# Kernel optimization log

Measured on AMD Instinct MI355X. Metric: run time of the kernel, lower is better.

Reference implementation:

```python
import jax, jax.numpy as jnp
import numpy as np

NEG = -1e30  # finite stand-in for -inf; exp underflows to exactly 0 in fp32


def setup_inputs() -> dict:
    key = jax.random.key(0)
    ks = jax.random.split(key, 8)
    B, L1, L2, D = 32, 2048, 512, 256
    x = jax.random.normal(ks[0], (B, L1, D), dtype=jnp.float32)
    y = jax.random.normal(ks[1], (B, L2, D), dtype=jnp.float32)
    x_mask = jax.random.randint(ks[2], (B, L1), 0, 2) > 0  # True = padding
    y_mask = jax.random.randint(ks[3], (B, L2), 0, 2) > 0
    w_x = jax.random.normal(ks[4], (D, 1), dtype=jnp.float32) * (1.0 / np.sqrt(D))
    w_y = jax.random.normal(ks[5], (D, 1), dtype=jnp.float32) * (1.0 / np.sqrt(D))
    w_dot = jax.random.normal(ks[6], (D, 1), dtype=jnp.float32) * (1.0 / np.sqrt(D))
    bias = jnp.zeros((1,), dtype=jnp.float32)
    return {"x": x, "y": y, "x_mask": x_mask, "y_mask": y_mask,
            "w_x": w_x, "w_y": w_y, "w_dot": w_dot, "bias": bias}


def reference(x, y, x_mask, y_mask, w_x, w_y, w_dot, bias):
    # trilinear BiDAF score: bias + x@w_x + y@w_y + sum_d x_d * y_d * w_dot_d
    # factorized -> no (B,L1,L2,D) intermediate, same math as xy.mm(w_dot)
    sx = x @ w_x                                    # (B, L1, 1)
    sy = jnp.swapaxes(y @ w_y, 1, 2)                # (B, 1, L2)
    sdot = jnp.einsum('bid,bjd->bij', x * w_dot[:, 0], y)  # (B, L1, L2)
    scores = bias[0] + sx + sy + sdot               # (B, L1, L2)
    scores = jnp.where(x_mask[:, :, None], NEG, scores)
    scores = jnp.where(y_mask[:, None, :], NEG, scores)

    alpha = jax.nn.softmax(scores, axis=2)          # (B, L1, L2)
    # torch code sets NaN rows (fully masked x positions) to 0
    valid_x = (~x_mask)[:, :, None].astype(x.dtype)
    alpha = alpha * valid_x
    c2q_attn = jnp.einsum('bij,bjd->bid', alpha, y)  # (B, L1, D)
    c2q_attn = c2q_attn * valid_x                    # maskzero on x padding

    beta = jax.nn.softmax(jnp.max(scores, axis=2), axis=1)  # (B, L1)
    q2c_attn = jnp.einsum('bi,bid->bd', beta, x)[:, None, :]  # (B, 1, D)

    return (c2q_attn, q2c_attn, x * c2q_attn)
```

## Files before the change

### kernel.cpp

```cpp
#include <hip/hip_runtime.h>
#include <stdint.h>

#define BB 32
#define L1 2048
#define L2 512
#define DD 256
#define NEGV -1e30f

typedef __attribute__((ext_vector_type(4))) float f32x4;
typedef __attribute__((ext_vector_type(8))) short bf16x8;
typedef __attribute__((ext_vector_type(4))) unsigned short u16x4;
typedef __attribute__((ext_vector_type(8))) unsigned short u16x8;

__device__ __forceinline__ unsigned short f2bf(float f) {
    unsigned int u = __float_as_uint(f);
    u += 0x7FFFu + ((u >> 16) & 1u);
    return (unsigned short)(u >> 16);
}

__global__ void prep(const float* __restrict__ y, const float* __restrict__ w_y,
                     unsigned short* __restrict__ ybf, unsigned short* __restrict__ yt,
                     float* __restrict__ sy) {
    __shared__ float tile[64][264];
    const int tid = threadIdx.x;
    const int lane = tid & 63;
    const int sub = tid >> 6;
    const int b = blockIdx.y;
    const int j0 = blockIdx.x * 64;
    const float* yb = y + ((size_t)b * L2 + j0) * DD;
    f32x4 wv = *(const f32x4*)(w_y + lane * 4);
    #pragma unroll
    for (int p = 0; p < 16; ++p) {
        int row = p * 4 + sub;
        f32x4 v = *(const f32x4*)(yb + (size_t)row * DD + lane * 4);
        *(f32x4*)&tile[row][lane * 4] = v;
        u16x4 o;
        o[0] = f2bf(v[0]); o[1] = f2bf(v[1]); o[2] = f2bf(v[2]); o[3] = f2bf(v[3]);
        *(u16x4*)(ybf + ((size_t)b * L2 + j0 + row) * DD + lane * 4) = o;
        float s = v[0]*wv[0] + v[1]*wv[1] + v[2]*wv[2] + v[3]*wv[3];
        #pragma unroll
        for (int off = 32; off; off >>= 1) s += __shfl_xor(s, off, 64);
        if (lane == 0) sy[b * L2 + j0 + row] = s;
    }
    __syncthreads();
    #pragma unroll
    for (int p = 0; p < 8; ++p) {
        int d = p * 32 + (tid >> 3);
        int jo = (tid & 7) * 8;
        u16x8 pk;
        #pragma unroll
        for (int jj = 0; jj < 8; ++jj) pk[jj] = f2bf(tile[jo + jj][d]);
        *(u16x8*)(yt + ((size_t)b * DD + d) * L2 + j0 + jo) = pk;
    }
}

__launch_bounds__(256, 2)
__global__ void attn_main(const float* __restrict__ x,
                          const unsigned short* __restrict__ ybf,
                          const unsigned short* __restrict__ yt,
                          const float* __restrict__ sy,
                          const float* __restrict__ w_x,
                          const float* __restrict__ w_dot,
                          const float* __restrict__ bias,
                          const int* __restrict__ x_mask,
                          const int* __restrict__ y_mask,
                          float* __restrict__ out0,
                          float* __restrict__ out2,
                          float* __restrict__ part,
                          float* __restrict__ MbA,
                          float* __restrict__ SeA) {
    __shared__ __align__(16) unsigned short big[32768];
    __shared__ float sxs[64];
    __shared__ int   xms[64];
    __shared__ float pmax[4][64];
    __shared__ float pz[4][64];

    const int tid = threadIdx.x;
    const int w = tid >> 6;
    const int lane = tid & 63;
    const int g = lane >> 4, c = lane & 15;

    const int wg = blockIdx.x;
    const int slot = wg >> 3;
    const int b = (wg & 7) * 4 + (slot >> 5);
    const int rowblk = slot & 31;
    const int i0 = rowblk * 64;

    const int arow = w * 16 + c;
    const float* xrow = x + ((size_t)(b * L1 + i0 + arow)) * DD;
    float sxpart = 0.f;
    #pragma unroll
    for (int kb = 0; kb < 8; ++kb) {
        int koff = kb * 32 + g * 8;
        f32x4 lo = *(const f32x4*)(xrow + koff);
        f32x4 hi = *(const f32x4*)(xrow + koff + 4);
        f32x4 wdlo = *(const f32x4*)(w_dot + koff);
        f32x4 wdhi = *(const f32x4*)(w_dot + koff + 4);
        f32x4 wxlo = *(const f32x4*)(w_x + koff);
        f32x4 wxhi = *(const f32x4*)(w_x + koff + 4);
        u16x8 a;
        #pragma unroll
        for (int e = 0; e < 4; ++e) {
            a[e]     = f2bf(lo[e] * wdlo[e]);
            a[e + 4] = f2bf(hi[e] * wdhi[e]);
            sxpart += lo[e] * wxlo[e] + hi[e] * wxhi[e];
        }
        int u = (kb * 4 + g) ^ (c & 7);
        *(u16x8*)((char*)big + arow * 512 + u * 16) = a;
    }
    sxpart += __shfl_xor(sxpart, 16, 64);
    sxpart += __shfl_xor(sxpart, 32, 64);
    if (g == 0) {
        sxs[arow] = sxpart + bias[0];
        xms[arow] = x_mask[b * L1 + i0 + arow];
    }
    __syncthreads();

    f32x4 S[4][8];
    #pragma unroll
    for (int mt = 0; mt < 4; ++mt)
        #pragma unroll
        for (int nt = 0; nt < 8; ++nt) S[mt][nt] = (f32x4){0.f, 0.f, 0.f, 0.f};

    const unsigned short* ybase = ybf + (size_t)b * L2 * DD;
    const int col0 = w * 128;
    #pragma unroll 2
    for (int ck = 0; ck < 8; ++ck) {
        bf16x8 bfr[8];
        #pragma unroll
        for (int nt = 0; nt < 8; ++nt)
            bfr[nt] = *(const bf16x8*)(ybase + (size_t)(col0 + nt * 16 + c) * DD + ck * 32 + g * 8);
        bf16x8 afr[4];
        #pragma unroll
        for (int mt = 0; mt < 4; ++mt) {
            int u = (ck * 4 + g) ^ (c & 7);
            afr[mt] = *(const bf16x8*)((char*)big + (mt * 16 + c) * 512 + u * 16);
        }
        #pragma unroll
        for (int mt = 0; mt < 4; ++mt)
            #pragma unroll
            for (int nt = 0; nt < 8; ++nt)
                S[mt][nt] = __builtin_amdgcn_mfma_f32_16x16x32_bf16(afr[mt], bfr[nt], S[mt][nt], 0, 0, 0);
    }

    float syv[8]; int ymv[8];
    #pragma unroll
    for (int nt = 0; nt < 8; ++nt) {
        syv[nt] = sy[b * L2 + col0 + nt * 16 + c];
        ymv[nt] = y_mask[b * L2 + col0 + nt * 16 + c];
    }
    float sxr[4][4]; int xmr[4][4];
    #pragma unroll
    for (int mt = 0; mt < 4; ++mt)
        #pragma unroll
        for (int r = 0; r < 4; ++r) {
            sxr[mt][r] = sxs[mt * 16 + 4 * g + r];
            xmr[mt][r] = xms[mt * 16 + 4 * g + r];
        }
    #pragma unroll
    for (int mt = 0; mt < 4; ++mt)
        #pragma unroll
        for (int nt = 0; nt < 8; ++nt)
            #pragma unroll
            for (int r = 0; r < 4; ++r) {
                float v = S[mt][nt][r] + sxr[mt][r] + syv[nt];
                if (ymv[nt]) v = NEGV;
                if (xmr[mt][r]) v = NEGV;
                S[mt][nt][r] = v;
            }

    float mrow[4][4];
    #pragma unroll
    for (int mt = 0; mt < 4; ++mt)
        #pragma unroll
        for (int r = 0; r < 4; ++r) {
            float pm = S[mt][0][r];
            #pragma unroll
            for (int nt = 1; nt < 8; ++nt) pm = fmaxf(pm, S[mt][nt][r]);
            pm = fmaxf(pm, __shfl_xor(pm, 1, 64));
            pm = fmaxf(pm, __shfl_xor(pm, 2, 64));
            pm = fmaxf(pm, __shfl_xor(pm, 4, 64));
            pm = fmaxf(pm, __shfl_xor(pm, 8, 64));
            if (c == 0) pmax[w][mt * 16 + 4 * g + r] = pm;
        }
    __syncthreads();
    #pragma unroll
    for (int mt = 0; mt < 4; ++mt)
        #pragma unroll
        for (int r = 0; r < 4; ++r) {
            int row = mt * 16 + 4 * g + r;
            mrow[mt][r] = fmaxf(fmaxf(pmax[0][row], pmax[1][row]),
                                fmaxf(pmax[2][row], pmax[3][row]));
        }
    #pragma unroll
    for (int mt = 0; mt < 4; ++mt)
        #pragma unroll
        for (int r = 0; r < 4; ++r) {
            float zp = 0.f;
            #pragma unroll
            for (int nt = 0; nt < 8; ++nt) {
                float e = __expf(S[mt][nt][r] - mrow[mt][r]);
                S[mt][nt][r] = e;
                zp += e;
            }
            zp += __shfl_xor(zp, 1, 64);
            zp += __shfl_xor(zp, 2, 64);
            zp += __shfl_xor(zp, 4, 64);
            zp += __shfl_xor(zp, 8, 64);
            if (c == 0) pz[w][mt * 16 + 4 * g + r] = zp;
        }
    __syncthreads();
    float zinv[4][4];
    #pragma unroll
    for (int mt = 0; mt < 4; ++mt)
        #pragma unroll
        for (int r = 0; r < 4; ++r) {
            int row = mt * 16 + 4 * g + r;
            zinv[mt][r] = 1.f / (pz[0][row] + pz[1][row] + pz[2][row] + pz[3][row]);
        }

    float Mb;
    {
        float t = mrow[0][0];
        #pragma unroll
        for (int mt = 0; mt < 4; ++mt)
            #pragma unroll
            for (int r = 0; r < 4; ++r) t = fmaxf(t, mrow[mt][r]);
        t = fmaxf(t, __shfl_xor(t, 16, 64));
        t = fmaxf(t, __shfl_xor(t, 32, 64));
        Mb = t;
    }
    float ev[4][4];
    float Se = 0.f;
    #pragma unroll
    for (int mt = 0; mt < 4; ++mt)
        #pragma unroll
        for (int r = 0; r < 4; ++r) {
            ev[mt][r] = __expf(mrow[mt][r] - Mb);
            Se += ev[mt][r];
        }
    Se += __shfl_xor(Se, 16, 64);
    Se += __shfl_xor(Se, 32, 64);
    if (tid == 0) {
        MbA[b * 32 + rowblk] = Mb;
        SeA[b * 32 + rowblk] = Se;
    }

    #pragma unroll
    for (int mt = 0; mt < 4; ++mt)
        #pragma unroll
        for (int nt = 0; nt < 8; ++nt)
            #pragma unroll
            for (int r = 0; r < 4; ++r) {
                int row = mt * 16 + 4 * g + r;
                int col = col0 + nt * 16 + c;
                *(unsigned short*)((char*)big + row * 1024 +
                                   (((col >> 3) ^ (row & 7)) * 16) + (col & 7) * 2)
                    = f2bf(S[mt][nt][r]);
            }
    __syncthreads();

    f32x4 o[4][4];
    #pragma unroll
    for (int mt = 0; mt < 4; ++mt)
        #pragma unroll
        for (int nt = 0; nt < 4; ++nt) o[mt][nt] = (f32x4){0.f, 0.f, 0.f, 0.f};
    const unsigned short* ytb = yt + (size_t)b * DD * L2;
    const int d0 = w * 64;
    #pragma unroll 4
    for (int kf = 0; kf < 16; ++kf) {
        bf16x8 bv[4];
        #pragma unroll
        for (int nt = 0; nt < 4; ++nt)
            bv[nt] = *(const bf16x8*)(ytb + (size_t)(d0 + nt * 16 + c) * L2 + kf * 32 + g * 8);
        bf16x8 av[4];
        #pragma unroll
        for (int mt = 0; mt < 4; ++mt) {
            int u = (kf * 4 + g) ^ (c & 7);
            av[mt] = *(const bf16x8*)((char*)big + (mt * 16 + c) * 1024 + u * 16);
        }
        #pragma unroll
        for (int mt = 0; mt < 4; ++mt)
            #pragma unroll
            for (int nt = 0; nt < 4; ++nt)
                o[mt][nt] = __builtin_amdgcn_mfma_f32_16x16x32_bf16(av[mt], bv[nt], o[mt][nt], 0, 0, 0);
    }

    const float* xb2 = x + ((size_t)b * L1 + i0) * DD;
    const size_t outb = ((size_t)b * L1 + i0) * DD;
    float eq[4] = {0.f, 0.f, 0.f, 0.f};
    #pragma unroll
    for (int mt = 0; mt < 4; ++mt)
        #pragma unroll
        for (int r = 0; r < 4; ++r) {
            int row = mt * 16 + 4 * g + r;
            float zi = zinv[mt][r];
            float ee = ev[mt][r];
            int xmv = xmr[mt][r];
            #pragma unroll
            for (int nt = 0; nt < 4; ++nt) {
                int d = d0 + nt * 16 + c;
                float xv = xb2[(size_t)row * DD + d];
                float cv = xmv ? 0.f : o[mt][nt][r] * zi;
                out0[outb + (size_t)row * DD + d] = cv;
                out2[outb + (size_t)row * DD + d] = xv * cv;
                eq[nt] += ee * xv;
            }
        }
    #pragma unroll
    for (int nt = 0; nt < 4; ++nt) {
        float v = eq[nt];
        v += __shfl_xor(v, 16, 64);
        v += __shfl_xor(v, 32, 64);
        if (g == 0) part[((size_t)(b * 32 + rowblk)) * DD + d0 + nt * 16 + c] = v;
    }
}

__global__ void q2c_combine(const float* __restrict__ part, const float* __restrict__ MbA,
                            const float* __restrict__ SeA, float* __restrict__ out1) {
    int b = blockIdx.x, d = threadIdx.x;
    float M = -3.0e38f;
    #pragma unroll
    for (int k = 0; k < 32; ++k) M = fmaxf(M, MbA[b * 32 + k]);
    float Z = 0.f, s = 0.f;
    #pragma unroll
    for (int k = 0; k < 32; ++k) {
        float wk = __expf(MbA[b * 32 + k] - M);
        Z += SeA[b * 32 + k] * wk;
        s += part[((size_t)(b * 32 + k)) * DD + d] * wk;
    }
    out1[b * DD + d] = s / Z;
}

extern "C" void kernel_launch(void* const* d_in, const int* in_sizes, int n_in,
                              void* d_out, int out_size, void* d_ws, size_t ws_size,
                              hipStream_t stream) {
    const float* x = (const float*)d_in[0];
    const float* y = (const float*)d_in[1];
    const int* x_mask = (const int*)d_in[2];
    const int* y_mask = (const int*)d_in[3];
    const float* w_x = (const float*)d_in[4];
    const float* w_y = (const float*)d_in[5];
    const float* w_dot = (const float*)d_in[6];
    const float* bias = (const float*)d_in[7];

    char* ws = (char*)d_ws;
    unsigned short* ybf = (unsigned short*)ws;
    unsigned short* yt  = (unsigned short*)(ws + 8388608);
    float* sy   = (float*)(ws + 16777216);
    float* part = (float*)(ws + 16842752);
    float* MbA  = (float*)(ws + 17891328);
    float* SeA  = (float*)(ws + 17895424);

    float* out0 = (float*)d_out;
    float* out1 = out0 + (size_t)BB * L1 * DD;
    float* out2 = out1 + (size_t)BB * DD;

    prep<<<dim3(L2 / 64, BB), 256, 0, stream>>>(y, w_y, ybf, yt, sy);
    attn_main<<<dim3(BB * L1 / 64), 256, 0, stream>>>(x, ybf, yt, sy, w_x, w_dot, bias,
                                                      x_mask, y_mask, out0, out2,
                                                      part, MbA, SeA);
    q2c_combine<<<dim3(BB), 256, 0, stream>>>(part, MbA, SeA, out1);
}
```

Before: 124.3 us.

## Halve attention row tile to 32 rows, use exp2 with pre-scaled scores

Shrinks each workgroup's row tile from 64 to 32, which halves the LDS footprint and the register accumulators. The launch-bounds occupancy hint goes from 2 to 3, the grid doubles, and q2c_combine now reduces over 64 partials. Scores are pre-scaled by log2(e) so the softmax can use the hardware exp2, and the masks are folded into the sx/sy bias terms as large negatives, replacing the per-element selects. The cost is that each workgroup reloads the full bf16 y tiles, so global/L2 traffic for y doubles, and the bf16 conversion now uses the library intrinsic.

```diff
diff --git a/kernel.cpp b/kernel.cpp
--- a/kernel.cpp
+++ b/kernel.cpp
@@ -1,21 +1,29 @@
 #include <hip/hip_runtime.h>
+#include <hip/hip_bf16.h>
 #include <stdint.h>
 
 #define BB 32
 #define L1 2048
 #define L2 512
 #define DD 256
-#define NEGV -1e30f
+#define L2E 1.4426950408889634f
+#define NEGS (-1.0e30f * 1.4426950408889634f)
+
+#if __has_builtin(__builtin_amdgcn_exp2f)
+#define EXP2(x) __builtin_amdgcn_exp2f(x)
+#else
+#define EXP2(x) exp2f(x)
+#endif
 
 typedef __attribute__((ext_vector_type(4))) float f32x4;
 typedef __attribute__((ext_vector_type(8))) short bf16x8;
 typedef __attribute__((ext_vector_type(4))) unsigned short u16x4;
 typedef __attribute__((ext_vector_type(8))) unsigned short u16x8;
 
-__device__ __forceinline__ unsigned short f2bf(float f) {
-    unsigned int u = __float_as_uint(f);
-    u += 0x7FFFu + ((u >> 16) & 1u);
-    return (unsigned short)(u >> 16);
+__device__ __forceinline__ unsigned short f2b(float f) {
+    union { __hip_bfloat16 h; unsigned short u; } cv;
+    cv.h = __float2bfloat16(f);
+    return cv.u;
 }
 
 __global__ void prep(const float* __restrict__ y, const float* __restrict__ w_y,
@@ -35,7 +43,7 @@
         f32x4 v = *(const f32x4*)(yb + (size_t)row * DD + lane * 4);
         *(f32x4*)&tile[row][lane * 4] = v;
         u16x4 o;
-        o[0] = f2bf(v[0]); o[1] = f2bf(v[1]); o[2] = f2bf(v[2]); o[3] = f2bf(v[3]);
+        o[0] = f2b(v[0]); o[1] = f2b(v[1]); o[2] = f2b(v[2]); o[3] = f2b(v[3]);
         *(u16x4*)(ybf + ((size_t)b * L2 + j0 + row) * DD + lane * 4) = o;
         float s = v[0]*wv[0] + v[1]*wv[1] + v[2]*wv[2] + v[3]*wv[3];
         #pragma unroll
@@ -49,12 +57,12 @@
         int jo = (tid & 7) * 8;
         u16x8 pk;
         #pragma unroll
-        for (int jj = 0; jj < 8; ++jj) pk[jj] = f2bf(tile[jo + jj][d]);
+        for (int jj = 0; jj < 8; ++jj) pk[jj] = f2b(tile[jo + jj][d]);
         *(u16x8*)(yt + ((size_t)b * DD + d) * L2 + j0 + jo) = pk;
     }
 }
 
-__launch_bounds__(256, 2)
+__launch_bounds__(256, 3)
 __global__ void attn_main(const float* __restrict__ x,
                           const unsigned short* __restrict__ ybf,
                           const unsigned short* __restrict__ yt,
@@ -69,11 +77,11 @@
                           float* __restrict__ part,
                           float* __restrict__ MbA,
                           float* __restrict__ SeA) {
-    __shared__ __align__(16) unsigned short big[32768];
-    __shared__ float sxs[64];
-    __shared__ int   xms[64];
-    __shared__ float pmax[4][64];
-    __shared__ float pz[4][64];
+    __shared__ __align__(16) unsigned short big[16384];
+    __shared__ float sxs[32];
+    __shared__ int   xms[32];
+    __shared__ float pmax[4][32];
+    __shared__ float pz[4][32];
 
     const int tid = threadIdx.x;
     const int w = tid >> 6;
@@ -82,96 +90,90 @@
 
     const int wg = blockIdx.x;
     const int slot = wg >> 3;
-    const int b = (wg & 7) * 4 + (slot >> 5);
-    const int rowblk = slot & 31;
-    const int i0 = rowblk * 64;
-
-    const int arow = w * 16 + c;
-    const float* xrow = x + ((size_t)(b * L1 + i0 + arow)) * DD;
-    float sxpart = 0.f;
-    #pragma unroll
-    for (int kb = 0; kb < 8; ++kb) {
-        int koff = kb * 32 + g * 8;
-        f32x4 lo = *(const f32x4*)(xrow + koff);
-        f32x4 hi = *(const f32x4*)(xrow + koff + 4);
-        f32x4 wdlo = *(const f32x4*)(w_dot + koff);
-        f32x4 wdhi = *(const f32x4*)(w_dot + koff + 4);
-        f32x4 wxlo = *(const f32x4*)(w_x + koff);
-        f32x4 wxhi = *(const f32x4*)(w_x + koff + 4);
-        u16x8 a;
-        #pragma unroll
-        for (int e = 0; e < 4; ++e) {
-            a[e]     = f2bf(lo[e] * wdlo[e]);
-            a[e + 4] = f2bf(hi[e] * wdhi[e]);
-            sxpart += lo[e] * wxlo[e] + hi[e] * wxhi[e];
-        }
-        int u = (kb * 4 + g) ^ (c & 7);
-        *(u16x8*)((char*)big + arow * 512 + u * 16) = a;
-    }
-    sxpart += __shfl_xor(sxpart, 16, 64);
-    sxpart += __shfl_xor(sxpart, 32, 64);
-    if (g == 0) {
-        sxs[arow] = sxpart + bias[0];
-        xms[arow] = x_mask[b * L1 + i0 + arow];
-    }
-    __syncthreads();
-
-    f32x4 S[4][8];
-    #pragma unroll
-    for (int mt = 0; mt < 4; ++mt)
+    const int b = (wg & 7) * 4 + (slot >> 6);
+    const int rowblk = slot & 63;
+    const int i0 = rowblk * 32;
+
+    {
+        const int arow = w * 8 + (lane >> 3);
+        const int chunk = lane & 7;
+        const float* xr = x + ((size_t)(b * L1 + i0 + arow)) * DD + chunk * 32;
+        const float* wdp = w_dot + chunk * 32;
+        const float* wxp = w_x + chunk * 32;
+        float sxp = 0.f;
+        #pragma unroll
+        for (int it = 0; it < 8; ++it) {
+            f32x4 xv = *(const f32x4*)(xr + it * 4);
+            f32x4 wdv = *(const f32x4*)(wdp + it * 4);
+            f32x4 wxv = *(const f32x4*)(wxp + it * 4);
+            u16x4 a;
+            #pragma unroll
+            for (int e = 0; e < 4; ++e) a[e] = f2b(xv[e] * wdv[e]);
+            sxp += xv[0]*wxv[0] + xv[1]*wxv[1] + xv[2]*wxv[2] + xv[3]*wxv[3];
+            int gr = chunk * 4 + (it >> 1);
+            *(u16x4*)((char*)big + arow * 512 + ((gr ^ (arow & 7)) << 4) + (it & 1) * 8) = a;
+        }
+        sxp += __shfl_xor(sxp, 1, 64);
+        sxp += __shfl_xor(sxp, 2, 64);
+        sxp += __shfl_xor(sxp, 4, 64);
+        if (chunk == 0) {
+            int xmv = x_mask[b * L1 + i0 + arow];
+            xms[arow] = xmv;
+            sxs[arow] = xmv ? NEGS : (sxp + bias[0]) * L2E;
+        }
+    }
+    __syncthreads();
+
+    f32x4 S[2][8];
+    #pragma unroll
+    for (int mt = 0; mt < 2; ++mt)
         #pragma unroll
         for (int nt = 0; nt < 8; ++nt) S[mt][nt] = (f32x4){0.f, 0.f, 0.f, 0.f};
 
     const unsigned short* ybase = ybf + (size_t)b * L2 * DD;
     const int col0 = w * 128;
-    #pragma unroll 2
+    #pragma unroll
     for (int ck = 0; ck < 8; ++ck) {
         bf16x8 bfr[8];
         #pragma unroll
         for (int nt = 0; nt < 8; ++nt)
             bfr[nt] = *(const bf16x8*)(ybase + (size_t)(col0 + nt * 16 + c) * DD + ck * 32 + g * 8);
-        bf16x8 afr[4];
-        #pragma unroll
-        for (int mt = 0; mt < 4; ++mt) {
-            int u = (ck * 4 + g) ^ (c & 7);
-            afr[mt] = *(const bf16x8*)((char*)big + (mt * 16 + c) * 512 + u * 16);
-        }
-        #pragma unroll
-        for (int mt = 0; mt < 4; ++mt)
+        bf16x8 afr[2];
+        #pragma unroll
+        for (int mt = 0; mt < 2; ++mt)
+            afr[mt] = *(const bf16x8*)((char*)big + (mt * 16 + c) * 512 + ((((ck * 4 + g)) ^ (c & 7)) << 4));
+        #pragma unroll
+        for (int mt = 0; mt < 2; ++mt)
             #pragma unroll
             for (int nt = 0; nt < 8; ++nt)
                 S[mt][nt] = __builtin_amdgcn_mfma_f32_16x16x32_bf16(afr[mt], bfr[nt], S[mt][nt], 0, 0, 0);
     }
 
-    float syv[8]; int ymv[8];
+    float syt[8];
     #pragma unroll
     for (int nt = 0; nt < 8; ++nt) {
-        syv[nt] = sy[b * L2 + col0 + nt * 16 + c];
-        ymv[nt] = y_mask[b * L2 + col0 + nt * 16 + c];
-    }
-    float sxr[4][4]; int xmr[4][4];
-    #pragma unroll
-    for (int mt = 0; mt < 4; ++mt)
+        float sv = sy[b * L2 + col0 + nt * 16 + c];
+        int ym = y_mask[b * L2 + col0 + nt * 16 + c];
+        syt[nt] = ym ? NEGS : sv * L2E;
+    }
+    float sxr[2][4]; int xmr[2][4];
+    #pragma unroll
+    for (int mt = 0; mt < 2; ++mt)
         #pragma unroll
         for (int r = 0; r < 4; ++r) {
             sxr[mt][r] = sxs[mt * 16 + 4 * g + r];
             xmr[mt][r] = xms[mt * 16 + 4 * g + r];
         }
     #pragma unroll
-    for (int mt = 0; mt < 4; ++mt)
+    for (int mt = 0; mt < 2; ++mt)
         #pragma unroll
         for (int nt = 0; nt < 8; ++nt)
             #pragma unroll
-            for (int r = 0; r < 4; ++r) {
-                float v = S[mt][nt][r] + sxr[mt][r] + syv[nt];
-                if (ymv[nt]) v = NEGV;
-                if (xmr[mt][r]) v = NEGV;
-                S[mt][nt][r] = v;
-            }
-
-    float mrow[4][4];
-    #pragma unroll
-    for (int mt = 0; mt < 4; ++mt)
+            for (int r = 0; r < 4; ++r)
+                S[mt][nt][r] = fmaf(S[mt][nt][r], L2E, sxr[mt][r]) + syt[nt];
+
+    #pragma unroll
+    for (int mt = 0; mt < 2; ++mt)
         #pragma unroll
         for (int r = 0; r < 4; ++r) {
             float pm = S[mt][0][r];
@@ -184,8 +186,9 @@
             if (c == 0) pmax[w][mt * 16 + 4 * g + r] = pm;
         }
     __syncthreads();
-    #pragma unroll
-    for (int mt = 0; mt < 4; ++mt)
+    float mrow[2][4];
+    #pragma unroll
+    for (int mt = 0; mt < 2; ++mt)
         #pragma unroll
         for (int r = 0; r < 4; ++r) {
             int row = mt * 16 + 4 * g + r;
@@ -193,13 +196,13 @@
                                 fmaxf(pmax[2][row], pmax[3][row]));
         }
     #pragma unroll
-    for (int mt = 0; mt < 4; ++mt)
+    for (int mt = 0; mt < 2; ++mt)
         #pragma unroll
         for (int r = 0; r < 4; ++r) {
             float zp = 0.f;
             #pragma unroll
             for (int nt = 0; nt < 8; ++nt) {
-                float e = __expf(S[mt][nt][r] - mrow[mt][r]);
+                float e = EXP2(S[mt][nt][r] - mrow[mt][r]);
                 S[mt][nt][r] = e;
                 zp += e;
             }
@@ -210,9 +213,9 @@
             if (c == 0) pz[w][mt * 16 + 4 * g + r] = zp;
         }
     __syncthreads();
-    float zinv[4][4];
-    #pragma unroll
-    for (int mt = 0; mt < 4; ++mt)
+    float zinv[2][4];
+    #pragma unroll
+    for (int mt = 0; mt < 2; ++mt)
         #pragma unroll
         for (int r = 0; r < 4; ++r) {
             int row = mt * 16 + 4 * g + r;
@@ -223,31 +226,31 @@
     {
         float t = mrow[0][0];
         #pragma unroll
-        for (int mt = 0; mt < 4; ++mt)
+        for (int mt = 0; mt < 2; ++mt)
             #pragma unroll
             for (int r = 0; r < 4; ++r) t = fmaxf(t, mrow[mt][r]);
         t = fmaxf(t, __shfl_xor(t, 16, 64));
         t = fmaxf(t, __shfl_xor(t, 32, 64));
         Mb = t;
     }
-    float ev[4][4];
+    float ev[2][4];
     float Se = 0.f;
     #pragma unroll
-    for (int mt = 0; mt < 4; ++mt)
-        #pragma unroll
-        for (int r = 0; r < 4; ++r) {
-            ev[mt][r] = __expf(mrow[mt][r] - Mb);
+    for (int mt = 0; mt < 2; ++mt)
+        #pragma unroll
+        for (int r = 0; r < 4; ++r) {
+            ev[mt][r] = EXP2(mrow[mt][r] - Mb);
             Se += ev[mt][r];
         }
     Se += __shfl_xor(Se, 16, 64);
     Se += __shfl_xor(Se, 32, 64);
     if (tid == 0) {
-        MbA[b * 32 + rowblk] = Mb;
-        SeA[b * 32 + rowblk] = Se;
-    }
-
-    #pragma unroll
-    for (int mt = 0; mt < 4; ++mt)
+        MbA[b * 64 + rowblk] = Mb;
+        SeA[b * 64 + rowblk] = Se;
+    }
+
+    #pragma unroll
+    for (int mt = 0; mt < 2; ++mt)
         #pragma unroll
         for (int nt = 0; nt < 8; ++nt)
             #pragma unroll
@@ -255,32 +258,30 @@
                 int row = mt * 16 + 4 * g + r;
                 int col = col0 + nt * 16 + c;
                 *(unsigned short*)((char*)big + row * 1024 +
-                                   (((col >> 3) ^ (row & 7)) * 16) + (col & 7) * 2)
-                    = f2bf(S[mt][nt][r]);
+                                   (((col >> 3) ^ (row & 7)) << 4) + (col & 7) * 2)
+                    = f2b(S[mt][nt][r]);
             }
     __syncthreads();
 
-    f32x4 o[4][4];
-    #pragma unroll
-    for (int mt = 0; mt < 4; ++mt)
+    f32x4 o[2][4];
+    #pragma unroll
+    for (int mt = 0; mt < 2; ++mt)
         #pragma unroll
         for (int nt = 0; nt < 4; ++nt) o[mt][nt] = (f32x4){0.f, 0.f, 0.f, 0.f};
     const unsigned short* ytb = yt + (size_t)b * DD * L2;
     const int d0 = w * 64;
-    #pragma unroll 4
+    #pragma unroll
     for (int kf = 0; kf < 16; ++kf) {
         bf16x8 bv[4];
         #pragma unroll
         for (int nt = 0; nt < 4; ++nt)
             bv[nt] = *(const bf16x8*)(ytb + (size_t)(d0 + nt * 16 + c) * L2 + kf * 32 + g * 8);
-        bf16x8 av[4];
-        #pragma unroll
-        for (int mt = 0; mt < 4; ++mt) {
-            int u = (kf * 4 + g) ^ (c & 7);
-            av[mt] = *(const bf16x8*)((char*)big + (mt * 16 + c) * 1024 + u * 16);
-        }
-        #pragma unroll
-        for (int mt = 0; mt < 4; ++mt)
+        bf16x8 av[2];
+        #pragma unroll
+        for (int mt = 0; mt < 2; ++mt)
+            av[mt] = *(const bf16x8*)((char*)big + (mt * 16 + c) * 1024 + ((((kf * 4 + g)) ^ (c & 7)) << 4));
+        #pragma unroll
+        for (int mt = 0; mt < 2; ++mt)
             #pragma unroll
             for (int nt = 0; nt < 4; ++nt)
                 o[mt][nt] = __builtin_amdgcn_mfma_f32_16x16x32_bf16(av[mt], bv[nt], o[mt][nt], 0, 0, 0);
@@ -290,7 +291,7 @@
     const size_t outb = ((size_t)b * L1 + i0) * DD;
     float eq[4] = {0.f, 0.f, 0.f, 0.f};
     #pragma unroll
-    for (int mt = 0; mt < 4; ++mt)
+    for (int mt = 0; mt < 2; ++mt)
         #pragma unroll
         for (int r = 0; r < 4; ++r) {
             int row = mt * 16 + 4 * g + r;
@@ -304,7 +305,7 @@
                 float cv = xmv ? 0.f : o[mt][nt][r] * zi;
                 out0[outb + (size_t)row * DD + d] = cv;
                 out2[outb + (size_t)row * DD + d] = xv * cv;
-                eq[nt] += ee * xv;
+                eq[nt] = fmaf(ee, xv, eq[nt]);
             }
         }
     #pragma unroll
@@ -312,7 +313,7 @@
         float v = eq[nt];
         v += __shfl_xor(v, 16, 64);
         v += __shfl_xor(v, 32, 64);
-        if (g == 0) part[((size_t)(b * 32 + rowblk)) * DD + d0 + nt * 16 + c] = v;
+        if (g == 0) part[((size_t)(b * 64 + rowblk)) * DD + d0 + nt * 16 + c] = v;
     }
 }
 
@@ -321,13 +322,13 @@
     int b = blockIdx.x, d = threadIdx.x;
     float M = -3.0e38f;
     #pragma unroll
-    for (int k = 0; k < 32; ++k) M = fmaxf(M, MbA[b * 32 + k]);
+    for (int k = 0; k < 64; ++k) M = fmaxf(M, MbA[b * 64 + k]);
     float Z = 0.f, s = 0.f;
-    #pragma unroll
-    for (int k = 0; k < 32; ++k) {
-        float wk = __expf(MbA[b * 32 + k] - M);
-        Z += SeA[b * 32 + k] * wk;
-        s += part[((size_t)(b * 32 + k)) * DD + d] * wk;
+    #pragma unroll 8
+    for (int k = 0; k < 64; ++k) {
+        float wk = exp2f(MbA[b * 64 + k] - M);
+        Z += SeA[b * 64 + k] * wk;
+        s += part[((size_t)(b * 64 + k)) * DD + d] * wk;
     }
     out1[b * DD + d] = s / Z;
 }
@@ -349,15 +350,15 @@
     unsigned short* yt  = (unsigned short*)(ws + 8388608);
     float* sy   = (float*)(ws + 16777216);
     float* part = (float*)(ws + 16842752);
-    float* MbA  = (float*)(ws + 17891328);
-    float* SeA  = (float*)(ws + 17895424);
+    float* MbA  = (float*)(ws + 18939904);
+    float* SeA  = (float*)(ws + 18948096);
 
     float* out0 = (float*)d_out;
     float* out1 = out0 + (size_t)BB * L1 * DD;
     float* out2 = out1 + (size_t)BB * DD;
 
     prep<<<dim3(L2 / 64, BB), 256, 0, stream>>>(y, w_y, ybf, yt, sy);
-    attn_main<<<dim3(BB * L1 / 64), 256, 0, stream>>>(x, ybf, yt, sy, w_x, w_dot, bias,
+    attn_main<<<dim3(BB * L1 / 32), 256, 0, stream>>>(x, ybf, yt, sy, w_x, w_dot, bias,
                                                       x_mask, y_mask, out0, out2,
                                                       part, MbA, SeA);
     q2c_combine<<<dim3(BB), 256, 0, stream>>>(part, MbA, SeA, out1);
```

Measured after the change: 182.2 us. 46.6% more time.
